# Optimization experiments

Hardware: AMD Instinct MI355X
Metric: run time of the kernel (lower is better)

The kernel has to match this reference:

```python
import jax, jax.numpy as jnp
import numpy as np

K_REGION = 32
C_CONTEXT = 128
CONF_THR = 0.5


def safe_normalize(x):
    return x / jnp.maximum(x.sum(axis=-1, keepdims=True), 1e-6)


def _geometry(mask_grid, h, w):
    # mask_grid: [B, K, h*w] -> per-mask bbox (x_min,y_min,x_max,y_max) + area, vectorized
    B, K, _ = mask_grid.shape
    m2 = mask_grid.reshape(B, K, h, w)
    present = m2 > 0.05
    rows = present.any(-1)  # [B,K,h]
    cols = present.any(-2)  # [B,K,w]
    yi = jnp.arange(h)
    xi = jnp.arange(w)
    y_min = jnp.min(jnp.where(rows, yi, h), axis=-1).astype(jnp.float32)
    y_max = jnp.max(jnp.where(rows, yi, -1), axis=-1).astype(jnp.float32)
    x_min = jnp.min(jnp.where(cols, xi, w), axis=-1).astype(jnp.float32)
    x_max = jnp.max(jnp.where(cols, xi, -1), axis=-1).astype(jnp.float32)
    hden = float(max(h - 1, 1))
    wden = float(max(w - 1, 1))
    area = present.astype(jnp.float32).mean(axis=(-1, -2))
    geom = jnp.stack([x_min / wden, y_min / hden, x_max / wden, y_max / hden, area], axis=-1)
    has_any = present.any(axis=(-1, -2))
    return jnp.where(has_any[..., None], geom, 0.0).astype(mask_grid.dtype)


def setup_inputs():
    key = jax.random.key(0)
    ks = jax.random.split(key, 16)
    B, N, D, M, Hm, Wm, Qd, Hd = 8, 576, 1024, 64, 384, 384, 4096, 1024
    inp = {}
    inp['patch_tokens'] = jax.random.normal(ks[0], (B, N, D), jnp.float32)
    inp['masks'] = jax.random.uniform(ks[1], (B, M, Hm, Wm), jnp.float32)
    inp['scores'] = jax.random.uniform(ks[2], (B, M), jnp.float32)
    inp['question_embed'] = jax.random.normal(ks[3], (B, Qd), jnp.float32)
    s = 0.02
    inp['W1'] = jax.random.normal(ks[4], (5, D), jnp.float32) * s
    inp['b1'] = jnp.zeros((D,), jnp.float32)
    inp['W2'] = jax.random.normal(ks[5], (D, D), jnp.float32) * s
    inp['b2'] = jnp.zeros((D,), jnp.float32)
    inp['Wv'] = jax.random.normal(ks[6], (D, Hd), jnp.float32) * s
    inp['bv'] = jnp.zeros((Hd,), jnp.float32)
    inp['Wp'] = jax.random.normal(ks[7], (1, Hd), jnp.float32) * s
    inp['bp'] = jnp.zeros((Hd,), jnp.float32)
    inp['Wq'] = jax.random.normal(ks[8], (Qd, Hd), jnp.float32) * s
    inp['bq'] = jnp.zeros((Hd,), jnp.float32)
    inp['Wo'] = jax.random.normal(ks[9], (Hd, 1), jnp.float32) * s
    inp['bo'] = jnp.zeros((1,), jnp.float32)
    inp['type_emb'] = jax.random.normal(ks[10], (3, D), jnp.float32) * s
    inp['patch_h'] = 24
    inp['patch_w'] = 24
    return inp


def reference(patch_tokens, masks, scores, question_embed, W1, b1, W2, b2,
              Wv, bv, Wp, bp, Wq, bq, Wo, bo, type_emb, patch_h, patch_w):
    B, N, D = patch_tokens.shape
    h, w = patch_h, patch_w
    M = masks.shape[1]

    grounding_valid = (masks.reshape(B, M, -1).sum(-1) > 0).any(-1)  # [B]

    order = jnp.argsort(-scores, axis=1)
    scores_s = jnp.take_along_axis(scores, order, axis=1)
    masks_s = jnp.take_along_axis(masks, order[:, :, None, None], axis=1)
    masks_k = masks_s[:, :K_REGION]
    scores_k = scores_s[:, :K_REGION]
    valid = scores_k >= CONF_THR
    masks_k = masks_k * valid[:, :, None, None].astype(masks_k.dtype)
    scores_k = jnp.where(valid, scores_k, 0.0)

    # MaskDownsampler: adaptive avg pool (exact: Hm,Wm divisible by h,w)
    Hm, Wm = masks_k.shape[-2:]
    fh, fw = Hm // h, Wm // w
    mg = masks_k.reshape(B, K_REGION, h, fh, w, fw).mean(axis=(3, 5)).reshape(B, K_REGION, h * w)

    uniform = jnp.full((B, K_REGION, N), 1.0 / N, dtype=patch_tokens.dtype)
    mg = jnp.where(grounding_valid[:, None, None], mg, uniform)
    scores_k = jnp.where(grounding_valid[:, None], scores_k, 1.0)

    # RegionPooler
    nm = safe_normalize(jnp.maximum(mg, 0.0))
    pooled = jnp.einsum('bkn,bnd->bkd', nm, patch_tokens)
    weighted = pooled * scores_k[..., None]
    geom = _geometry(mg, h, w)  # [B,K,5]
    g = jax.nn.silu(geom @ W1 + b1) @ W2 + b2
    region_tokens = weighted + g

    patch_prior = (mg * scores_k[..., None]).sum(axis=1)
    patch_prior = safe_normalize(jnp.maximum(patch_prior, 0.0))
    patch_prior = jnp.where(grounding_valid[:, None], patch_prior, jnp.full_like(patch_prior, 1.0 / N))

    # RoutingScorer
    hid = jnp.tanh(patch_tokens @ Wv + bv
                   + patch_prior[:, :, None] @ Wp + bp
                   + (question_embed @ Wq + bq)[:, None, :])
    routing_scores = (hid @ Wo + bo)[..., 0]  # [B,N]
    routing_weights = jax.nn.softmax(routing_scores, axis=-1)

    top_k = min(C_CONTEXT, N)
    _, sel_idx = jax.lax.top_k(routing_scores, top_k)
    context_tokens = jnp.take_along_axis(patch_tokens, sel_idx[:, :, None], axis=1)
    sel_mask = jnp.zeros((B, N), patch_tokens.dtype).at[jnp.arange(B)[:, None], sel_idx].set(1.0)

    # BackgroundPooler
    residual = jnp.maximum(1.0 - sel_mask, 0.0)
    residual = residual / jnp.maximum(residual.sum(-1, keepdims=True), 1e-6)
    bg = jnp.einsum('bn,bnd->bd', residual, patch_tokens)

    region_tokens = region_tokens + type_emb[0][None, None, :]
    context_tokens = context_tokens + type_emb[1][None, None, :]
    background_token = bg[:, None, :] + type_emb[2][None, None, :]
    visual_tokens = jnp.concatenate([region_tokens, context_tokens, background_token], axis=1)

    return (visual_tokens, region_tokens, context_tokens, background_token,
            patch_prior, routing_weights, sel_idx, grounding_valid)
```

## Files before the change

### kernel.cpp

```cpp
#include <hip/hip_runtime.h>
#include <math.h>

typedef long long I64;

#define NB    8
#define NTOK  576
#define DIM   1024
#define NMASK 64
#define HMASK 384
#define WMASK 384
#define QDIM  4096
#define HDIM  1024
#define KREG  32
#define CCTX  128
#define GH    24
#define GW    24
#define GNUM  576

#define OFF_VIS 0
#define OFF_REG 1318912
#define OFF_CTX 1581056
#define OFF_BG  2629632
#define OFF_PP  2637824
#define OFF_RW  2642432
#define OFF_SEL 2647040
#define OFF_GV  2648064

#define WS_BS   0
#define WS_NMAT 294912
#define WS_SCK  442368
#define WS_H1   442624
#define WS_Q    704768
#define WS_Q2   712960
#define WS_GV   721152
#define WS_PP   721160
#define WS_CS   725768
#define WS_RSP  733960

#define QBLK      256
#define BS_BLOCKS (NB * NMASK * 24)

__global__ __launch_bounds__(384) void k_bsq(const float* __restrict__ masks,
                                             const float* __restrict__ qe,
                                             const float* __restrict__ Wq,
                                             const float* __restrict__ bq,
                                             float* __restrict__ ws) {
  int gid = blockIdx.x;
  int t = threadIdx.x;
  __shared__ float shm[2048 + 6 * 64];
  if (gid >= QBLK) {
    int gid2 = gid - QBLK;
    int yband = gid2 % 24;
    int bm = gid2 / 24;
    float (*sm)[96] = (float(*)[96])shm;
    const float4* src = (const float4*)(masks + (I64)bm * (HMASK * WMASK) + (I64)yband * 16 * WMASK);
    float4 s4 = src[t];
    float4 v1 = src[t + 384];
    float4 v2 = src[t + 768];
    float4 v3 = src[t + 1152];
    s4.x += v1.x; s4.y += v1.y; s4.z += v1.z; s4.w += v1.w;
    s4.x += v2.x; s4.y += v2.y; s4.z += v2.z; s4.w += v2.w;
    s4.x += v3.x; s4.y += v3.y; s4.z += v3.z; s4.w += v3.w;
    float s = (s4.x + s4.y) + (s4.z + s4.w);
    sm[t / 96][t % 96] = s;
    __syncthreads();
    if (t < 24) {
      float tt = 0.f;
      #pragma unroll
      for (int rg = 0; rg < 4; ++rg)
        #pragma unroll
        for (int c = 0; c < 4; ++c) tt += sm[rg][t * 4 + c];
      ws[WS_BS + (I64)bm * GNUM + yband * 24 + t] = tt;
    }
  } else {
    int b = gid >> 5;
    int r = gid & 31;
    int qb = r >> 1;
    int ih = r & 1;
    int base = ih * 2048;
    float* qs = shm;
    float (*sp)[64] = (float(*)[64])(shm + 2048);
    {
      const float4* s4 = (const float4*)(qe + (I64)b * QDIM + base);
      float4 v = s4[t];
      *(float4*)&qs[t * 4] = v;
      if (t < 128) {
        float4 v2 = s4[t + 384];
        *(float4*)&qs[(t + 384) * 4] = v2;
      }
    }
    __syncthreads();
    int dl = t & 63, ig = t >> 6;
    int d = qb * 64 + dl;
    const float* wq = Wq + d;
    float a0 = 0.f, a1 = 0.f, a2 = 0.f, a3 = 0.f;
    float a4 = 0.f, a5 = 0.f, a6 = 0.f, a7 = 0.f;
    int i = ig;
    for (; i + 42 < 2048; i += 48) {
      a0 = fmaf(qs[i],      wq[(I64)(base + i) * HDIM],      a0);
      a1 = fmaf(qs[i + 6],  wq[(I64)(base + i + 6) * HDIM],  a1);
      a2 = fmaf(qs[i + 12], wq[(I64)(base + i + 12) * HDIM], a2);
      a3 = fmaf(qs[i + 18], wq[(I64)(base + i + 18) * HDIM], a3);
      a4 = fmaf(qs[i + 24], wq[(I64)(base + i + 24) * HDIM], a4);
      a5 = fmaf(qs[i + 30], wq[(I64)(base + i + 30) * HDIM], a5);
      a6 = fmaf(qs[i + 36], wq[(I64)(base + i + 36) * HDIM], a6);
      a7 = fmaf(qs[i + 42], wq[(I64)(base + i + 42) * HDIM], a7);
    }
    for (; i < 2048; i += 6)
      a0 = fmaf(qs[i], wq[(I64)(base + i) * HDIM], a0);
    sp[ig][dl] = ((a0 + a1) + (a2 + a3)) + ((a4 + a5) + (a6 + a7));
    __syncthreads();
    if (t < 64) {
      float s2 = ((sp[0][t] + sp[1][t]) + (sp[2][t] + sp[3][t])) + (sp[4][t] + sp[5][t]);
      int dd = qb * 64 + t;
      float outv = s2 + (ih ? 0.f : bq[dd]);
      ws[(ih ? WS_Q2 : WS_Q) + (I64)b * HDIM + dd] = outv;
    }
  }
}

#define MGPAD 580
__global__ __launch_bounds__(256) void k_perbatch(
    const float* __restrict__ bs, const float* __restrict__ scores,
    const float* __restrict__ W1, const float* __restrict__ b1,
    float* __restrict__ ws, float* __restrict__ out) {
  int b = blockIdx.x;
  int t = threadIdx.x;
  __shared__ float s_mg[KREG][MGPAD];
  __shared__ float s_sc[NMASK];
  __shared__ float s_msum[NMASK];
  __shared__ int   s_order[NMASK];
  __shared__ float s_sck[KREG];
  __shared__ int   s_valid[KREG];
  __shared__ int   s_midx[KREG];
  __shared__ float s_rowsum[KREG];
  __shared__ float s_pp[GNUM];
  __shared__ float s_geom[KREG][5];
  __shared__ float s_red[64];
  __shared__ int   s_gv;
  __shared__ float s_ppsum;

  {
    int m = t >> 2, q = t & 3;
    const float4* p = (const float4*)(bs + ((I64)b * NMASK + m) * GNUM) + q * 36;
    float s = 0.f;
    #pragma unroll 4
    for (int j = 0; j < 36; ++j) {
      float4 v = p[j];
      s += v.x; s += v.y; s += v.z; s += v.w;
    }
    s += __shfl_xor(s, 1);
    s += __shfl_xor(s, 2);
    if (q == 0) s_msum[m] = s;
  }
  if (t < NMASK) s_sc[t] = scores[b * NMASK + t];
  __syncthreads();
  if (t == 0) {
    int g = 0;
    for (int m = 0; m < NMASK; ++m) g |= (s_msum[m] > 0.f) ? 1 : 0;
    s_gv = g;
  }
  if (t < NMASK) {
    float v = s_sc[t];
    int r = 0;
    for (int j = 0; j < NMASK; ++j) {
      float vj = s_sc[j];
      r += (vj > v) || (vj == v && j < t);
    }
    s_order[r] = t;
  }
  __syncthreads();
  const int gv = s_gv;
  if (t < KREG) {
    int m = s_order[t];
    float sc = s_sc[m];
    int valid = (sc >= 0.5f) ? 1 : 0;
    s_midx[t] = m;
    s_valid[t] = valid;
    float sck = gv ? (valid ? sc : 0.f) : 1.f;
    s_sck[t] = sck;
    ws[WS_SCK + b * KREG + t] = sck;
  }
  __syncthreads();
  {
    int k = t >> 3, sub = t & 7;
    const float inv256 = 1.f / 256.f;
    const float invN = 1.f / 576.f;
    float scale = gv ? (s_valid[k] ? inv256 : 0.f) : 0.f;
    float addv  = gv ? 0.f : invN;
    const float4* src = (const float4*)(bs + ((I64)b * NMASK + s_midx[k]) * GNUM) + sub * 18;
    float* dst = &s_mg[k][sub * 72];
    #pragma unroll 3
    for (int j = 0; j < 18; ++j) {
      float4 v = src[j];
      v.x = v.x * scale + addv;
      v.y = v.y * scale + addv;
      v.z = v.z * scale + addv;
      v.w = v.w * scale + addv;
      *(float4*)(dst + j * 4) = v;
    }
  }
  __syncthreads();
  {
    int k = t >> 3, sub = t & 7;
    float part = 0.f;
    for (int n = sub; n < GNUM; n += 8) part += fmaxf(s_mg[k][n], 0.f);
    part += __shfl_xor(part, 1);
    part += __shfl_xor(part, 2);
    part += __shfl_xor(part, 4);
    if (sub == 0) s_rowsum[k] = part;
  }
  __syncthreads();
  for (int idx = t; idx < KREG * GNUM; idx += 256) {
    int k = idx / GNUM, n = idx - k * GNUM;
    float v = fmaxf(s_mg[k][n], 0.f);
    ws[WS_NMAT + ((I64)b * KREG + k) * GNUM + n] = v / fmaxf(s_rowsum[k], 1e-6f);
  }
  for (int n = t; n < GNUM; n += 256) {
    float raw = 0.f;
    #pragma unroll
    for (int k = 0; k < KREG; ++k) raw = fmaf(s_mg[k][n], s_sck[k], raw);
    s_pp[n] = fmaxf(raw, 0.f);
  }
  __syncthreads();
  if (t < 64) {
    float s = 0.f;
    for (int n = t; n < GNUM; n += 64) s += s_pp[n];
    s_red[t] = s;
  }
  __syncthreads();
  if (t == 0) {
    float s = 0.f;
    for (int i = 0; i < 64; ++i) s += s_red[i];
    s_ppsum = s;
  }
  __syncthreads();
  {
    const float invN = 1.f / 576.f;
    float den = fmaxf(s_ppsum, 1e-6f);
    for (int n = t; n < GNUM; n += 256) {
      float v = gv ? (s_pp[n] / den) : invN;
      ws[WS_PP + b * GNUM + n] = v;
      out[OFF_PP + b * GNUM + n] = v;
    }
  }
  {
    int k = t >> 3, sub = t & 7;
    unsigned colmask = 0u;
    int ymin = GH, ymax = -1, cnt = 0;
    #pragma unroll
    for (int yy = 0; yy < 3; ++yy) {
      int y = sub * 3 + yy;
      unsigned rowm = 0u;
      for (int x = 0; x < GW; ++x)
        if (s_mg[k][y * GW + x] > 0.05f) rowm |= (1u << x);
      if (rowm) { if (y < ymin) ymin = y; if (y > ymax) ymax = y; }
      colmask |= rowm;
      cnt += __popc(rowm);
    }
    #pragma unroll
    for (int off = 1; off < 8; off <<= 1) {
      colmask |= (unsigned)__shfl_xor((int)colmask, off);
      cnt += __shfl_xor(cnt, off);
      int o1 = __shfl_xor(ymin, off); ymin = (o1 < ymin) ? o1 : ymin;
      int o2 = __shfl_xor(ymax, off); ymax = (o2 > ymax) ? o2 : ymax;
    }
    if (sub == 0) {
      float g0, g1, g2, g3, g4;
      if (cnt > 0) {
        int xmin = __ffs(colmask) - 1;
        int xmax = 31 - __clz(colmask);
        g0 = (float)xmin / 23.f;
        g1 = (float)ymin / 23.f;
        g2 = (float)xmax / 23.f;
        g3 = (float)ymax / 23.f;
        g4 = (float)cnt / 576.f;
      } else { g0 = g1 = g2 = g3 = g4 = 0.f; }
      s_geom[k][0] = g0; s_geom[k][1] = g1; s_geom[k][2] = g2;
      s_geom[k][3] = g3; s_geom[k][4] = g4;
    }
  }
  __syncthreads();
  for (int idx = t; idx < KREG * HDIM; idx += 256) {
    int k = idx >> 10, j = idx & 1023;
    float x = 0.f;
    #pragma unroll
    for (int i = 0; i < 5; ++i) x += s_geom[k][i] * W1[i * HDIM + j];
    x += b1[j];
    float sg = 1.f / (1.f + expf(-x));
    ws[WS_H1 + ((I64)b * KREG + k) * HDIM + j] = x * sg;
  }
  if (t == 0) {
    float g = gv ? 1.f : 0.f;
    ws[WS_GV + b] = g;
    out[OFF_GV + b] = g;
  }
}

__global__ __launch_bounds__(512) void k_region(
    const float* __restrict__ pt, const float* __restrict__ W2,
    const float* __restrict__ b2, const float* __restrict__ te,
    float* __restrict__ ws, float* __restrict__ out) {
  int blk = blockIdx.x;
  int b = blk >> 6, kg = (blk >> 3) & 7, dg = blk & 7;
  int t = threadIdx.x;
  int dl = t & 127;
  int qh = t >> 7;
  int d = dg * 128 + dl;
  const float* nmb = ws + WS_NMAT + ((I64)b * KREG + kg * 4) * GNUM;
  const float* h1b = ws + WS_H1 + ((I64)b * KREG + kg * 4) * HDIM;
  float accP[4] = {0, 0, 0, 0};
  float accG[4] = {0, 0, 0, 0};
  float accS = 0.f;
  int n0 = qh * 144, n1 = n0 + 144;
  for (int n = n0; n < n1; ++n) {
    float p = pt[((I64)b * NTOK + n) * DIM + d];
    accS += p;
    #pragma unroll
    for (int kk = 0; kk < 4; ++kk)
      accP[kk] = fmaf(nmb[kk * GNUM + n], p, accP[kk]);
  }
  int j0 = qh * 256, j1 = j0 + 256;
  for (int j = j0; j < j1; ++j) {
    float wv = W2[(I64)j * DIM + d];
    #pragma unroll
    for (int kk = 0; kk < 4; ++kk)
      accG[kk] = fmaf(h1b[kk * HDIM + j], wv, accG[kk]);
  }
  __shared__ float cmbP[4][4][128];
  __shared__ float cmbG[4][4][128];
  __shared__ float cmbS[4][128];
  #pragma unroll
  for (int kk = 0; kk < 4; ++kk) {
    cmbP[qh][kk][dl] = accP[kk];
    cmbG[qh][kk][dl] = accG[kk];
  }
  cmbS[qh][dl] = accS;
  __syncthreads();
  if (qh == 0) {
    float bb = b2[d], t0 = te[d];
    #pragma unroll
    for (int kk = 0; kk < 4; ++kk) {
      int k = kg * 4 + kk;
      float P = (cmbP[0][kk][dl] + cmbP[1][kk][dl]) + (cmbP[2][kk][dl] + cmbP[3][kk][dl]);
      float G = (cmbG[0][kk][dl] + cmbG[1][kk][dl]) + (cmbG[2][kk][dl] + cmbG[3][kk][dl]);
      float val = P * ws[WS_SCK + b * KREG + k] + G + bb + t0;
      out[OFF_REG + ((I64)b * KREG + k) * DIM + d] = val;
      out[OFF_VIS + ((I64)b * 161 + k) * DIM + d] = val;
    }
    if (kg == 0)
      ws[WS_CS + (I64)b * DIM + d] =
          (cmbS[0][dl] + cmbS[1][dl]) + (cmbS[2][dl] + cmbS[3][dl]);
  }
}

#define PA 36
#define PW 164
__global__ __launch_bounds__(256, 1) void k_hid4(
    const float* __restrict__ pt, const float* __restrict__ Wv,
    const float* __restrict__ bv, const float* __restrict__ Wp,
    const float* __restrict__ bp, const float* __restrict__ Wo,
    float* __restrict__ ws) {
  int blk = blockIdx.x;
  int b = blk >> 5;
  int r = blk & 31;
  int tokTile = r >> 3;
  int colTile = r & 7;
  int n0 = tokTile * 144;
  int col0 = colTile * 128;
  int t = threadIdx.x;
  int trow = t >> 4;
  int tcol = t & 15;

  __shared__ float sA[2][144][PA];
  __shared__ float sW[2][32][PW];

  float acc[9][8];
  #pragma unroll
  for (int i = 0; i < 9; ++i)
    #pragma unroll
    for (int j = 0; j < 8; ++j) acc[i][j] = 0.f;

  int a_row0 = t >> 3, a_kq0 = t & 7;
  int a_row1 = (t + 256) >> 3, a_kq1 = t & 7;
  int a_row2 = (t + 512) >> 3;
  int a_row3 = (t + 768) >> 3;
  int a_row4 = (t + 1024) >> 3;
  int w_k0 = t >> 5, w_c = t & 31;

  float4 pa0, pa1, pa2, pa3, pa4;
  float4 pw0, pw1, pw2, pw3;

  const float* ptb = pt + (I64)(b * NTOK + n0) * DIM;
  const float* wvb = Wv + col0;

  {
    pa0 = *(const float4*)&ptb[(I64)a_row0 * DIM + a_kq0 * 4];
    pa1 = *(const float4*)&ptb[(I64)a_row1 * DIM + a_kq1 * 4];
    pa2 = *(const float4*)&ptb[(I64)a_row2 * DIM + a_kq1 * 4];
    pa3 = *(const float4*)&ptb[(I64)a_row3 * DIM + a_kq1 * 4];
    if (t < 128) pa4 = *(const float4*)&ptb[(I64)a_row4 * DIM + a_kq1 * 4];
    pw0 = *(const float4*)&wvb[(I64)(w_k0 +  0) * HDIM + w_c * 4];
    pw1 = *(const float4*)&wvb[(I64)(w_k0 +  8) * HDIM + w_c * 4];
    pw2 = *(const float4*)&wvb[(I64)(w_k0 + 16) * HDIM + w_c * 4];
    pw3 = *(const float4*)&wvb[(I64)(w_k0 + 24) * HDIM + w_c * 4];
    *(float4*)&sA[0][a_row0][a_kq0 * 4] = pa0;
    *(float4*)&sA[0][a_row1][a_kq1 * 4] = pa1;
    *(float4*)&sA[0][a_row2][a_kq1 * 4] = pa2;
    *(float4*)&sA[0][a_row3][a_kq1 * 4] = pa3;
    if (t < 128) *(float4*)&sA[0][a_row4][a_kq1 * 4] = pa4;
    *(float4*)&sW[0][w_k0 +  0][w_c * 4] = pw0;
    *(float4*)&sW[0][w_k0 +  8][w_c * 4] = pw1;
    *(float4*)&sW[0][w_k0 + 16][w_c * 4] = pw2;
    *(float4*)&sW[0][w_k0 + 24][w_c * 4] = pw3;
  }

  for (int s = 0; s < 32; ++s) {
    __syncthreads();
    if (s + 1 < 32) {
      int k0 = (s + 1) * 32;
      pa0 = *(const float4*)&ptb[(I64)a_row0 * DIM + k0 + a_kq0 * 4];
      pa1 = *(const float4*)&ptb[(I64)a_row1 * DIM + k0 + a_kq1 * 4];
      pa2 = *(const float4*)&ptb[(I64)a_row2 * DIM + k0 + a_kq1 * 4];
      pa3 = *(const float4*)&ptb[(I64)a_row3 * DIM + k0 + a_kq1 * 4];
      if (t < 128) pa4 = *(const float4*)&ptb[(I64)a_row4 * DIM + k0 + a_kq1 * 4];
      pw0 = *(const float4*)&wvb[(I64)(k0 + w_k0 +  0) * HDIM + w_c * 4];
      pw1 = *(const float4*)&wvb[(I64)(k0 + w_k0 +  8) * HDIM + w_c * 4];
      pw2 = *(const float4*)&wvb[(I64)(k0 + w_k0 + 16) * HDIM + w_c * 4];
      pw3 = *(const float4*)&wvb[(I64)(k0 + w_k0 + 24) * HDIM + w_c * 4];
    }
    int cur = s & 1;
    #pragma unroll 2
    for (int kk4 = 0; kk4 < 8; ++kk4) {
      float4 af[9];
      #pragma unroll
      for (int i = 0; i < 9; ++i)
        af[i] = *(const float4*)&sA[cur][trow * 9 + i][kk4 * 4];
      float4 w0[4], w1[4];
      #pragma unroll
      for (int m = 0; m < 4; ++m) {
        w0[m] = *(const float4*)&sW[cur][kk4 * 4 + m][tcol * 4];
        w1[m] = *(const float4*)&sW[cur][kk4 * 4 + m][64 + tcol * 4];
      }
      #pragma unroll
      for (int i = 0; i < 9; ++i) {
        #pragma unroll
        for (int m = 0; m < 4; ++m) {
          float a = ((const float*)&af[i])[m];
          acc[i][0] = fmaf(a, w0[m].x, acc[i][0]);
          acc[i][1] = fmaf(a, w0[m].y, acc[i][1]);
          acc[i][2] = fmaf(a, w0[m].z, acc[i][2]);
          acc[i][3] = fmaf(a, w0[m].w, acc[i][3]);
          acc[i][4] = fmaf(a, w1[m].x, acc[i][4]);
          acc[i][5] = fmaf(a, w1[m].y, acc[i][5]);
          acc[i][6] = fmaf(a, w1[m].z, acc[i][6]);
          acc[i][7] = fmaf(a, w1[m].w, acc[i][7]);
        }
      }
    }
    if (s + 1 < 32) {
      int nxt = (s + 1) & 1;
      *(float4*)&sA[nxt][a_row0][a_kq0 * 4] = pa0;
      *(float4*)&sA[nxt][a_row1][a_kq1 * 4] = pa1;
      *(float4*)&sA[nxt][a_row2][a_kq1 * 4] = pa2;
      *(float4*)&sA[nxt][a_row3][a_kq1 * 4] = pa3;
      if (t < 128) *(float4*)&sA[nxt][a_row4][a_kq1 * 4] = pa4;
      *(float4*)&sW[nxt][w_k0 +  0][w_c * 4] = pw0;
      *(float4*)&sW[nxt][w_k0 +  8][w_c * 4] = pw1;
      *(float4*)&sW[nxt][w_k0 + 16][w_c * 4] = pw2;
      *(float4*)&sW[nxt][w_k0 + 24][w_c * 4] = pw3;
    }
  }

  int ca = col0 + tcol * 4;
  int cb = col0 + 64 + tcol * 4;
  float4 bvA = *(const float4*)&bv[ca], bvB = *(const float4*)&bv[cb];
  float4 bpA = *(const float4*)&bp[ca], bpB = *(const float4*)&bp[cb];
  float4 wpA = *(const float4*)&Wp[ca], wpB = *(const float4*)&Wp[cb];
  float4 woA = *(const float4*)&Wo[ca], woB = *(const float4*)&Wo[cb];
  float4 qaA = *(const float4*)&ws[WS_Q  + (I64)b * HDIM + ca];
  float4 qaB = *(const float4*)&ws[WS_Q  + (I64)b * HDIM + cb];
  float4 qbA = *(const float4*)&ws[WS_Q2 + (I64)b * HDIM + ca];
  float4 qbB = *(const float4*)&ws[WS_Q2 + (I64)b * HDIM + cb];
  float bvv[8] = {bvA.x, bvA.y, bvA.z, bvA.w, bvB.x, bvB.y, bvB.z, bvB.w};
  float bpv[8] = {bpA.x, bpA.y, bpA.z, bpA.w, bpB.x, bpB.y, bpB.z, bpB.w};
  float wpv[8] = {wpA.x, wpA.y, wpA.z, wpA.w, wpB.x, wpB.y, wpB.z, wpB.w};
  float wov[8] = {woA.x, woA.y, woA.z, woA.w, woB.x, woB.y, woB.z, woB.w};
  float qv[8]  = {qaA.x + qbA.x, qaA.y + qbA.y, qaA.z + qbA.z, qaA.w + qbA.w,
                  qaB.x + qbB.x, qaB.y + qbB.y, qaB.z + qbB.z, qaB.w + qbB.w};
  float partial[9];
  #pragma unroll
  for (int i = 0; i < 9; ++i) {
    float ppv = ws[WS_PP + b * GNUM + n0 + trow * 9 + i];
    float s = 0.f;
    #pragma unroll
    for (int j = 0; j < 8; ++j) {
      float pre = acc[i][j] + bvv[j] + bpv[j] + qv[j] + ppv * wpv[j];
      s = fmaf(wov[j], tanhf(pre), s);
    }
    partial[i] = s;
  }
  #pragma unroll
  for (int i = 0; i < 9; ++i) {
    float p = partial[i];
    p += __shfl_xor(p, 1);
    p += __shfl_xor(p, 2);
    p += __shfl_xor(p, 4);
    p += __shfl_xor(p, 8);
    partial[i] = p;
  }
  if (tcol == 0) {
    #pragma unroll
    for (int i = 0; i < 9; ++i)
      ws[WS_RSP + ((I64)b * NTOK + n0 + trow * 9 + i) * 8 + colTile] = partial[i];
  }
}

__global__ __launch_bounds__(576) void k_soft(const float* __restrict__ bo,
                                              float* __restrict__ ws, float* __restrict__ out) {
  int b = blockIdx.x, t = threadIdx.x;
  __shared__ float s_rs[NTOK];
  __shared__ float s_w[9];
  __shared__ float s_max, s_sum;
  {
    const float4* p = (const float4*)(ws + WS_RSP + ((I64)b * NTOK + t) * 8);
    float4 v0 = p[0], v1 = p[1];
    s_rs[t] = bo[0] + (((v0.x + v0.y) + (v0.z + v0.w)) + ((v1.x + v1.y) + (v1.z + v1.w)));
  }
  __syncthreads();
  float v = s_rs[t];
  int r = 0;
  for (int j = 0; j < NTOK; ++j) {
    float vj = s_rs[j];
    r += (vj > v) || (vj == v && j < t);
  }
  float m = v;
  for (int off = 1; off < 64; off <<= 1) m = fmaxf(m, __shfl_xor(m, off));
  if ((t & 63) == 0) s_w[t >> 6] = m;
  __syncthreads();
  if (t == 0) {
    float mm = s_w[0];
    for (int i = 1; i < 9; ++i) mm = fmaxf(mm, s_w[i]);
    s_max = mm;
  }
  __syncthreads();
  float e = expf(v - s_max);
  float s = e;
  for (int off = 1; off < 64; off <<= 1) s += __shfl_xor(s, off);
  if ((t & 63) == 0) s_w[t >> 6] = s;
  __syncthreads();
  if (t == 0) {
    float ss = 0.f;
    for (int i = 0; i < 9; ++i) ss += s_w[i];
    s_sum = ss;
  }
  __syncthreads();
  out[OFF_RW + b * NTOK + t] = e / s_sum;
  if (r < CCTX) out[OFF_SEL + b * CCTX + r] = (float)t;
}

__global__ __launch_bounds__(256) void k_post(const float* __restrict__ pt, const float* __restrict__ te,
                                              const float* __restrict__ ws, const float* __restrict__ outr,
                                              float* __restrict__ out) {
  int rr = blockIdx.x, b = blockIdx.y;
  int d = threadIdx.x * 4;
  if (rr < CCTX) {
    int idx = (int)outr[OFF_SEL + b * CCTX + rr];
    float4 v = *(const float4*)&pt[((I64)b * NTOK + idx) * DIM + d];
    float4 e = *(const float4*)&te[DIM + d];
    v.x += e.x; v.y += e.y; v.z += e.z; v.w += e.w;
    *(float4*)&out[OFF_CTX + ((I64)b * CCTX + rr) * DIM + d] = v;
    *(float4*)&out[OFF_VIS + ((I64)b * 161 + KREG + rr) * DIM + d] = v;
  } else {
    float4 s = *(const float4*)&ws[WS_CS + (I64)b * DIM + d];
    for (int r = 0; r < CCTX; ++r) {
      int idx = (int)outr[OFF_SEL + b * CCTX + r];
      float4 v = *(const float4*)&pt[((I64)b * NTOK + idx) * DIM + d];
      s.x -= v.x; s.y -= v.y; s.z -= v.z; s.w -= v.w;
    }
    const float rinv = 1.f / 448.f;
    float4 e = *(const float4*)&te[2 * DIM + d];
    float4 o;
    o.x = s.x * rinv + e.x; o.y = s.y * rinv + e.y;
    o.z = s.z * rinv + e.z; o.w = s.w * rinv + e.w;
    *(float4*)&out[OFF_BG + (I64)b * DIM + d] = o;
    *(float4*)&out[OFF_VIS + ((I64)b * 161 + 160) * DIM + d] = o;
  }
}

extern "C" void kernel_launch(void* const* d_in, const int* in_sizes, int n_in,
                              void* d_out, int out_size, void* d_ws, size_t ws_size,
                              hipStream_t stream) {
  (void)in_sizes; (void)n_in; (void)out_size; (void)ws_size;
  const float* pt     = (const float*)d_in[0];
  const float* masks  = (const float*)d_in[1];
  const float* scores = (const float*)d_in[2];
  const float* qe     = (const float*)d_in[3];
  const float* W1     = (const float*)d_in[4];
  const float* b1     = (const float*)d_in[5];
  const float* W2     = (const float*)d_in[6];
  const float* b2     = (const float*)d_in[7];
  const float* Wv     = (const float*)d_in[8];
  const float* bv     = (const float*)d_in[9];
  const float* Wp     = (const float*)d_in[10];
  const float* bp     = (const float*)d_in[11];
  const float* Wq     = (const float*)d_in[12];
  const float* bq     = (const float*)d_in[13];
  const float* Wo     = (const float*)d_in[14];
  const float* bo     = (const float*)d_in[15];
  const float* te     = (const float*)d_in[16];
  float* out = (float*)d_out;
  float* ws  = (float*)d_ws;

  k_bsq<<<dim3(QBLK + BS_BLOCKS), dim3(384), 0, stream>>>(masks, qe, Wq, bq, ws);
  k_perbatch<<<dim3(NB), dim3(256), 0, stream>>>(ws + WS_BS, scores, W1, b1, ws, out);
  k_region<<<dim3(512), dim3(512), 0, stream>>>(pt, W2, b2, te, ws, out);
  k_hid4<<<dim3(256), dim3(256), 0, stream>>>(pt, Wv, bv, Wp, bp, Wo, ws);
  k_soft<<<dim3(NB), dim3(576), 0, stream>>>(bo, ws, out);
  k_post<<<dim3(CCTX + 1, NB), dim3(256), 0, stream>>>(pt, te, ws, out, out);
}
```

Measured before the change: 343.2 us.

## Fold hidden GEMM into mask/query megakernel and split tanh epilogue into region kernel

The Wv GEMM moves into the first launch alongside the mask band sums and the question projection. It no longer depends on patch_prior, so it can overlap those independent stages, and it writes the raw hidden matrix to workspace. The tanh/Wo epilogue, which needs patch_prior, is appended as extra blocks in the region kernel, and softmax then reads finished routing scores. The GEMM drops LDS double buffering so three blocks can fit per CU, and the background pooling gather is split across four thread groups. The cost is an extra ~19MB hidden-state write and read through workspace.

```diff
diff --git a/kernel.cpp b/kernel.cpp
--- a/kernel.cpp
+++ b/kernel.cpp
@@ -35,86 +35,183 @@
 #define WS_GV   721152
 #define WS_PP   721160
 #define WS_CS   725768
-#define WS_RSP  733960
+#define WS_RS   733960
+#define WS_HID  775432
+#define WS_END  5494024
 
 #define QBLK      256
 #define BS_BLOCKS (NB * NMASK * 24)
-
-__global__ __launch_bounds__(384) void k_bsq(const float* __restrict__ masks,
-                                             const float* __restrict__ qe,
-                                             const float* __restrict__ Wq,
-                                             const float* __restrict__ bq,
-                                             float* __restrict__ ws) {
+#define HIDBLK    256
+#define MEGA_GRID (HIDBLK + QBLK + BS_BLOCKS)
+
+__global__ __launch_bounds__(256, 3) void k_mega(
+    const float* __restrict__ masks, const float* __restrict__ qe,
+    const float* __restrict__ Wq, const float* __restrict__ bq,
+    const float* __restrict__ pt, const float* __restrict__ Wv,
+    float* __restrict__ ws) {
   int gid = blockIdx.x;
   int t = threadIdx.x;
-  __shared__ float shm[2048 + 6 * 64];
-  if (gid >= QBLK) {
-    int gid2 = gid - QBLK;
-    int yband = gid2 % 24;
-    int bm = gid2 / 24;
-    float (*sm)[96] = (float(*)[96])shm;
-    const float4* src = (const float4*)(masks + (I64)bm * (HMASK * WMASK) + (I64)yband * 16 * WMASK);
-    float4 s4 = src[t];
-    float4 v1 = src[t + 384];
-    float4 v2 = src[t + 768];
-    float4 v3 = src[t + 1152];
-    s4.x += v1.x; s4.y += v1.y; s4.z += v1.z; s4.w += v1.w;
-    s4.x += v2.x; s4.y += v2.y; s4.z += v2.z; s4.w += v2.w;
-    s4.x += v3.x; s4.y += v3.y; s4.z += v3.z; s4.w += v3.w;
-    float s = (s4.x + s4.y) + (s4.z + s4.w);
-    sm[t / 96][t % 96] = s;
-    __syncthreads();
-    if (t < 24) {
-      float tt = 0.f;
-      #pragma unroll
-      for (int rg = 0; rg < 4; ++rg)
-        #pragma unroll
-        for (int c = 0; c < 4; ++c) tt += sm[rg][t * 4 + c];
-      ws[WS_BS + (I64)bm * GNUM + yband * 24 + t] = tt;
-    }
-  } else {
+  __shared__ __align__(16) float smem[10432];
+
+  if (gid < HIDBLK) {
     int b = gid >> 5;
     int r = gid & 31;
-    int qb = r >> 1;
-    int ih = r & 1;
+    int tokTile = r >> 3;
+    int colTile = r & 7;
+    int n0 = tokTile * 144;
+    int col0 = colTile * 128;
+    int trow = t >> 4;
+    int tcol = t & 15;
+
+    float (*sA)[36]  = (float(*)[36])smem;
+    float (*sW)[164] = (float(*)[164])(smem + 5184);
+
+    float acc[9][8];
+    #pragma unroll
+    for (int i = 0; i < 9; ++i)
+      #pragma unroll
+      for (int j = 0; j < 8; ++j) acc[i][j] = 0.f;
+
+    int a_row0 = t >> 3, a_kq = t & 7;
+    int a_row1 = (t + 256) >> 3;
+    int a_row2 = (t + 512) >> 3;
+    int a_row3 = (t + 768) >> 3;
+    int a_row4 = (t + 1024) >> 3;
+    int w_k0 = t >> 5, w_c = t & 31;
+
+    const float* ptb = pt + (I64)(b * NTOK + n0) * DIM;
+    const float* wvb = Wv + col0;
+
+    float4 pa0, pa1, pa2, pa3, pa4 = {0,0,0,0};
+    float4 pw0, pw1, pw2, pw3;
+
+    pa0 = *(const float4*)&ptb[(I64)a_row0 * DIM + a_kq * 4];
+    pa1 = *(const float4*)&ptb[(I64)a_row1 * DIM + a_kq * 4];
+    pa2 = *(const float4*)&ptb[(I64)a_row2 * DIM + a_kq * 4];
+    pa3 = *(const float4*)&ptb[(I64)a_row3 * DIM + a_kq * 4];
+    if (t < 128) pa4 = *(const float4*)&ptb[(I64)a_row4 * DIM + a_kq * 4];
+    pw0 = *(const float4*)&wvb[(I64)(w_k0 +  0) * HDIM + w_c * 4];
+    pw1 = *(const float4*)&wvb[(I64)(w_k0 +  8) * HDIM + w_c * 4];
+    pw2 = *(const float4*)&wvb[(I64)(w_k0 + 16) * HDIM + w_c * 4];
+    pw3 = *(const float4*)&wvb[(I64)(w_k0 + 24) * HDIM + w_c * 4];
+
+    for (int s = 0; s < 32; ++s) {
+      __syncthreads();
+      *(float4*)&sA[a_row0][a_kq * 4] = pa0;
+      *(float4*)&sA[a_row1][a_kq * 4] = pa1;
+      *(float4*)&sA[a_row2][a_kq * 4] = pa2;
+      *(float4*)&sA[a_row3][a_kq * 4] = pa3;
+      if (t < 128) *(float4*)&sA[a_row4][a_kq * 4] = pa4;
+      *(float4*)&sW[w_k0 +  0][w_c * 4] = pw0;
+      *(float4*)&sW[w_k0 +  8][w_c * 4] = pw1;
+      *(float4*)&sW[w_k0 + 16][w_c * 4] = pw2;
+      *(float4*)&sW[w_k0 + 24][w_c * 4] = pw3;
+      __syncthreads();
+      if (s + 1 < 32) {
+        int k0 = (s + 1) * 32;
+        pa0 = *(const float4*)&ptb[(I64)a_row0 * DIM + k0 + a_kq * 4];
+        pa1 = *(const float4*)&ptb[(I64)a_row1 * DIM + k0 + a_kq * 4];
+        pa2 = *(const float4*)&ptb[(I64)a_row2 * DIM + k0 + a_kq * 4];
+        pa3 = *(const float4*)&ptb[(I64)a_row3 * DIM + k0 + a_kq * 4];
+        if (t < 128) pa4 = *(const float4*)&ptb[(I64)a_row4 * DIM + k0 + a_kq * 4];
+        pw0 = *(const float4*)&wvb[(I64)(k0 + w_k0 +  0) * HDIM + w_c * 4];
+        pw1 = *(const float4*)&wvb[(I64)(k0 + w_k0 +  8) * HDIM + w_c * 4];
+        pw2 = *(const float4*)&wvb[(I64)(k0 + w_k0 + 16) * HDIM + w_c * 4];
+        pw3 = *(const float4*)&wvb[(I64)(k0 + w_k0 + 24) * HDIM + w_c * 4];
+      }
+      __builtin_amdgcn_s_setprio(1);
+      #pragma unroll 2
+      for (int kk4 = 0; kk4 < 8; ++kk4) {
+        float4 af[9];
+        #pragma unroll
+        for (int i = 0; i < 9; ++i)
+          af[i] = *(const float4*)&sA[trow * 9 + i][kk4 * 4];
+        float4 w0[4], w1[4];
+        #pragma unroll
+        for (int m = 0; m < 4; ++m) {
+          w0[m] = *(const float4*)&sW[kk4 * 4 + m][tcol * 4];
+          w1[m] = *(const float4*)&sW[kk4 * 4 + m][64 + tcol * 4];
+        }
+        #pragma unroll
+        for (int i = 0; i < 9; ++i) {
+          #pragma unroll
+          for (int m = 0; m < 4; ++m) {
+            float a = ((const float*)&af[i])[m];
+            acc[i][0] = fmaf(a, w0[m].x, acc[i][0]);
+            acc[i][1] = fmaf(a, w0[m].y, acc[i][1]);
+            acc[i][2] = fmaf(a, w0[m].z, acc[i][2]);
+            acc[i][3] = fmaf(a, w0[m].w, acc[i][3]);
+            acc[i][4] = fmaf(a, w1[m].x, acc[i][4]);
+            acc[i][5] = fmaf(a, w1[m].y, acc[i][5]);
+            acc[i][6] = fmaf(a, w1[m].z, acc[i][6]);
+            acc[i][7] = fmaf(a, w1[m].w, acc[i][7]);
+          }
+        }
+      }
+      __builtin_amdgcn_s_setprio(0);
+    }
+    float* hid = ws + WS_HID + ((I64)b * NTOK + n0) * HDIM;
+    #pragma unroll
+    for (int i = 0; i < 9; ++i) {
+      int row = trow * 9 + i;
+      float4 va = {acc[i][0], acc[i][1], acc[i][2], acc[i][3]};
+      float4 vb = {acc[i][4], acc[i][5], acc[i][6], acc[i][7]};
+      *(float4*)&hid[(I64)row * HDIM + col0 + tcol * 4] = va;
+      *(float4*)&hid[(I64)row * HDIM + col0 + 64 + tcol * 4] = vb;
+    }
+  } else if (gid < HIDBLK + QBLK) {
+    int g = gid - HIDBLK;
+    int b = g >> 5, r = g & 31;
+    int qb = r >> 1, ih = r & 1;
     int base = ih * 2048;
-    float* qs = shm;
-    float (*sp)[64] = (float(*)[64])(shm + 2048);
-    {
-      const float4* s4 = (const float4*)(qe + (I64)b * QDIM + base);
-      float4 v = s4[t];
-      *(float4*)&qs[t * 4] = v;
-      if (t < 128) {
-        float4 v2 = s4[t + 384];
-        *(float4*)&qs[(t + 384) * 4] = v2;
-      }
-    }
+    float* qs = smem;
+    float (*sp)[64] = (float(*)[64])(smem + 2048);
+    const float4* s4 = (const float4*)(qe + (I64)b * QDIM + base);
+    *(float4*)&qs[t * 4] = s4[t];
+    *(float4*)&qs[(t + 256) * 4] = s4[t + 256];
     __syncthreads();
     int dl = t & 63, ig = t >> 6;
     int d = qb * 64 + dl;
     const float* wq = Wq + d;
     float a0 = 0.f, a1 = 0.f, a2 = 0.f, a3 = 0.f;
     float a4 = 0.f, a5 = 0.f, a6 = 0.f, a7 = 0.f;
-    int i = ig;
-    for (; i + 42 < 2048; i += 48) {
+    for (int i = ig; i < 2048; i += 32) {
       a0 = fmaf(qs[i],      wq[(I64)(base + i) * HDIM],      a0);
-      a1 = fmaf(qs[i + 6],  wq[(I64)(base + i + 6) * HDIM],  a1);
-      a2 = fmaf(qs[i + 12], wq[(I64)(base + i + 12) * HDIM], a2);
-      a3 = fmaf(qs[i + 18], wq[(I64)(base + i + 18) * HDIM], a3);
-      a4 = fmaf(qs[i + 24], wq[(I64)(base + i + 24) * HDIM], a4);
-      a5 = fmaf(qs[i + 30], wq[(I64)(base + i + 30) * HDIM], a5);
-      a6 = fmaf(qs[i + 36], wq[(I64)(base + i + 36) * HDIM], a6);
-      a7 = fmaf(qs[i + 42], wq[(I64)(base + i + 42) * HDIM], a7);
-    }
-    for (; i < 2048; i += 6)
-      a0 = fmaf(qs[i], wq[(I64)(base + i) * HDIM], a0);
+      a1 = fmaf(qs[i + 4],  wq[(I64)(base + i + 4) * HDIM],  a1);
+      a2 = fmaf(qs[i + 8],  wq[(I64)(base + i + 8) * HDIM],  a2);
+      a3 = fmaf(qs[i + 12], wq[(I64)(base + i + 12) * HDIM], a3);
+      a4 = fmaf(qs[i + 16], wq[(I64)(base + i + 16) * HDIM], a4);
+      a5 = fmaf(qs[i + 20], wq[(I64)(base + i + 20) * HDIM], a5);
+      a6 = fmaf(qs[i + 24], wq[(I64)(base + i + 24) * HDIM], a6);
+      a7 = fmaf(qs[i + 28], wq[(I64)(base + i + 28) * HDIM], a7);
+    }
     sp[ig][dl] = ((a0 + a1) + (a2 + a3)) + ((a4 + a5) + (a6 + a7));
     __syncthreads();
     if (t < 64) {
-      float s2 = ((sp[0][t] + sp[1][t]) + (sp[2][t] + sp[3][t])) + (sp[4][t] + sp[5][t]);
+      float s2 = (sp[0][t] + sp[1][t]) + (sp[2][t] + sp[3][t]);
       int dd = qb * 64 + t;
-      float outv = s2 + (ih ? 0.f : bq[dd]);
-      ws[(ih ? WS_Q2 : WS_Q) + (I64)b * HDIM + dd] = outv;
+      ws[(ih ? WS_Q2 : WS_Q) + (I64)b * HDIM + dd] = s2 + (ih ? 0.f : bq[dd]);
+    }
+  } else {
+    int g = gid - (HIDBLK + QBLK);
+    int yband = g % 24;
+    int bm = g / 24;
+    float (*sm)[96] = (float(*)[96])smem;
+    const float4* src = (const float4*)(masks + (I64)bm * (HMASK * WMASK) + (I64)yband * 16 * WMASK);
+    #pragma unroll
+    for (int j = 0; j < 6; ++j) {
+      int f = t + 256 * j;
+      float4 v = src[f];
+      sm[f / 96][f % 96] = (v.x + v.y) + (v.z + v.w);
+    }
+    __syncthreads();
+    if (t < 24) {
+      float tt = 0.f;
+      #pragma unroll
+      for (int rr = 0; rr < 16; ++rr)
+        #pragma unroll
+        for (int c = 0; c < 4; ++c) tt += sm[rr][t * 4 + c];
+      ws[WS_BS + (I64)bm * GNUM + yband * 24 + t] = tt;
     }
   }
 }
@@ -297,236 +394,103 @@
   }
 }
 
-__global__ __launch_bounds__(512) void k_region(
+__global__ __launch_bounds__(512) void k_regepi(
     const float* __restrict__ pt, const float* __restrict__ W2,
     const float* __restrict__ b2, const float* __restrict__ te,
+    const float* __restrict__ bv, const float* __restrict__ bp,
+    const float* __restrict__ Wp, const float* __restrict__ Wo,
+    const float* __restrict__ bo,
     float* __restrict__ ws, float* __restrict__ out) {
   int blk = blockIdx.x;
-  int b = blk >> 6, kg = (blk >> 3) & 7, dg = blk & 7;
   int t = threadIdx.x;
-  int dl = t & 127;
-  int qh = t >> 7;
-  int d = dg * 128 + dl;
-  const float* nmb = ws + WS_NMAT + ((I64)b * KREG + kg * 4) * GNUM;
-  const float* h1b = ws + WS_H1 + ((I64)b * KREG + kg * 4) * HDIM;
-  float accP[4] = {0, 0, 0, 0};
-  float accG[4] = {0, 0, 0, 0};
-  float accS = 0.f;
-  int n0 = qh * 144, n1 = n0 + 144;
-  for (int n = n0; n < n1; ++n) {
-    float p = pt[((I64)b * NTOK + n) * DIM + d];
-    accS += p;
-    #pragma unroll
-    for (int kk = 0; kk < 4; ++kk)
-      accP[kk] = fmaf(nmb[kk * GNUM + n], p, accP[kk]);
-  }
-  int j0 = qh * 256, j1 = j0 + 256;
-  for (int j = j0; j < j1; ++j) {
-    float wv = W2[(I64)j * DIM + d];
-    #pragma unroll
-    for (int kk = 0; kk < 4; ++kk)
-      accG[kk] = fmaf(h1b[kk * HDIM + j], wv, accG[kk]);
-  }
-  __shared__ float cmbP[4][4][128];
-  __shared__ float cmbG[4][4][128];
-  __shared__ float cmbS[4][128];
-  #pragma unroll
-  for (int kk = 0; kk < 4; ++kk) {
-    cmbP[qh][kk][dl] = accP[kk];
-    cmbG[qh][kk][dl] = accG[kk];
-  }
-  cmbS[qh][dl] = accS;
-  __syncthreads();
-  if (qh == 0) {
-    float bb = b2[d], t0 = te[d];
+  if (blk < 512) {
+    int b = blk >> 6, kg = (blk >> 3) & 7, dg = blk & 7;
+    int dl = t & 127;
+    int qh = t >> 7;
+    int d = dg * 128 + dl;
+    const float* nmb = ws + WS_NMAT + ((I64)b * KREG + kg * 4) * GNUM;
+    const float* h1b = ws + WS_H1 + ((I64)b * KREG + kg * 4) * HDIM;
+    float accP[4] = {0, 0, 0, 0};
+    float accG[4] = {0, 0, 0, 0};
+    float accS = 0.f;
+    int n0 = qh * 144, n1 = n0 + 144;
+    for (int n = n0; n < n1; ++n) {
+      float p = pt[((I64)b * NTOK + n) * DIM + d];
+      accS += p;
+      #pragma unroll
+      for (int kk = 0; kk < 4; ++kk)
+        accP[kk] = fmaf(nmb[kk * GNUM + n], p, accP[kk]);
+    }
+    int j0 = qh * 256, j1 = j0 + 256;
+    for (int j = j0; j < j1; ++j) {
+      float wv = W2[(I64)j * DIM + d];
+      #pragma unroll
+      for (int kk = 0; kk < 4; ++kk)
+        accG[kk] = fmaf(h1b[kk * HDIM + j], wv, accG[kk]);
+    }
+    __shared__ float cmbP[4][4][128];
+    __shared__ float cmbG[4][4][128];
+    __shared__ float cmbS[4][128];
     #pragma unroll
     for (int kk = 0; kk < 4; ++kk) {
-      int k = kg * 4 + kk;
-      float P = (cmbP[0][kk][dl] + cmbP[1][kk][dl]) + (cmbP[2][kk][dl] + cmbP[3][kk][dl]);
-      float G = (cmbG[0][kk][dl] + cmbG[1][kk][dl]) + (cmbG[2][kk][dl] + cmbG[3][kk][dl]);
-      float val = P * ws[WS_SCK + b * KREG + k] + G + bb + t0;
-      out[OFF_REG + ((I64)b * KREG + k) * DIM + d] = val;
-      out[OFF_VIS + ((I64)b * 161 + k) * DIM + d] = val;
-    }
-    if (kg == 0)
-      ws[WS_CS + (I64)b * DIM + d] =
-          (cmbS[0][dl] + cmbS[1][dl]) + (cmbS[2][dl] + cmbS[3][dl]);
+      cmbP[qh][kk][dl] = accP[kk];
+      cmbG[qh][kk][dl] = accG[kk];
+    }
+    cmbS[qh][dl] = accS;
+    __syncthreads();
+    if (qh == 0) {
+      float bb = b2[d], t0 = te[d];
+      #pragma unroll
+      for (int kk = 0; kk < 4; ++kk) {
+        int k = kg * 4 + kk;
+        float P = (cmbP[0][kk][dl] + cmbP[1][kk][dl]) + (cmbP[2][kk][dl] + cmbP[3][kk][dl]);
+        float G = (cmbG[0][kk][dl] + cmbG[1][kk][dl]) + (cmbG[2][kk][dl] + cmbG[3][kk][dl]);
+        float val = P * ws[WS_SCK + b * KREG + k] + G + bb + t0;
+        out[OFF_REG + ((I64)b * KREG + k) * DIM + d] = val;
+        out[OFF_VIS + ((I64)b * 161 + k) * DIM + d] = val;
+      }
+      if (kg == 0)
+        ws[WS_CS + (I64)b * DIM + d] =
+            (cmbS[0][dl] + cmbS[1][dl]) + (cmbS[2][dl] + cmbS[3][dl]);
+    }
+  } else {
+    int g = (blk - 512) * 32 + (t >> 4);
+    int l = t & 15;
+    int b = g / NTOK, n = g % NTOK;
+    const float* hid = ws + WS_HID + (I64)g * HDIM;
+    const float* q1 = ws + WS_Q + (I64)b * HDIM;
+    const float* q2 = ws + WS_Q2 + (I64)b * HDIM;
+    float ppv = ws[WS_PP + b * GNUM + n];
+    float ssum = 0.f;
+    #pragma unroll 4
+    for (int j = 0; j < 16; ++j) {
+      int c = l * 64 + j * 4;
+      float4 h4 = *(const float4*)&hid[c];
+      float4 b4 = *(const float4*)&bv[c];
+      float4 p4 = *(const float4*)&bp[c];
+      float4 w4 = *(const float4*)&Wp[c];
+      float4 o4 = *(const float4*)&Wo[c];
+      float4 qa = *(const float4*)&q1[c];
+      float4 qb = *(const float4*)&q2[c];
+      ssum = fmaf(o4.x, tanhf(h4.x + b4.x + p4.x + qa.x + qb.x + ppv * w4.x), ssum);
+      ssum = fmaf(o4.y, tanhf(h4.y + b4.y + p4.y + qa.y + qb.y + ppv * w4.y), ssum);
+      ssum = fmaf(o4.z, tanhf(h4.z + b4.z + p4.z + qa.z + qb.z + ppv * w4.z), ssum);
+      ssum = fmaf(o4.w, tanhf(h4.w + b4.w + p4.w + qa.w + qb.w + ppv * w4.w), ssum);
+    }
+    ssum += __shfl_xor(ssum, 1);
+    ssum += __shfl_xor(ssum, 2);
+    ssum += __shfl_xor(ssum, 4);
+    ssum += __shfl_xor(ssum, 8);
+    if (l == 0) ws[WS_RS + g] = ssum + bo[0];
   }
 }
 
-#define PA 36
-#define PW 164
-__global__ __launch_bounds__(256, 1) void k_hid4(
-    const float* __restrict__ pt, const float* __restrict__ Wv,
-    const float* __restrict__ bv, const float* __restrict__ Wp,
-    const float* __restrict__ bp, const float* __restrict__ Wo,
-    float* __restrict__ ws) {
-  int blk = blockIdx.x;
-  int b = blk >> 5;
-  int r = blk & 31;
-  int tokTile = r >> 3;
-  int colTile = r & 7;
-  int n0 = tokTile * 144;
-  int col0 = colTile * 128;
-  int t = threadIdx.x;
-  int trow = t >> 4;
-  int tcol = t & 15;
-
-  __shared__ float sA[2][144][PA];
-  __shared__ float sW[2][32][PW];
-
-  float acc[9][8];
-  #pragma unroll
-  for (int i = 0; i < 9; ++i)
-    #pragma unroll
-    for (int j = 0; j < 8; ++j) acc[i][j] = 0.f;
-
-  int a_row0 = t >> 3, a_kq0 = t & 7;
-  int a_row1 = (t + 256) >> 3, a_kq1 = t & 7;
-  int a_row2 = (t + 512) >> 3;
-  int a_row3 = (t + 768) >> 3;
-  int a_row4 = (t + 1024) >> 3;
-  int w_k0 = t >> 5, w_c = t & 31;
-
-  float4 pa0, pa1, pa2, pa3, pa4;
-  float4 pw0, pw1, pw2, pw3;
-
-  const float* ptb = pt + (I64)(b * NTOK + n0) * DIM;
-  const float* wvb = Wv + col0;
-
-  {
-    pa0 = *(const float4*)&ptb[(I64)a_row0 * DIM + a_kq0 * 4];
-    pa1 = *(const float4*)&ptb[(I64)a_row1 * DIM + a_kq1 * 4];
-    pa2 = *(const float4*)&ptb[(I64)a_row2 * DIM + a_kq1 * 4];
-    pa3 = *(const float4*)&ptb[(I64)a_row3 * DIM + a_kq1 * 4];
-    if (t < 128) pa4 = *(const float4*)&ptb[(I64)a_row4 * DIM + a_kq1 * 4];
-    pw0 = *(const float4*)&wvb[(I64)(w_k0 +  0) * HDIM + w_c * 4];
-    pw1 = *(const float4*)&wvb[(I64)(w_k0 +  8) * HDIM + w_c * 4];
-    pw2 = *(const float4*)&wvb[(I64)(w_k0 + 16) * HDIM + w_c * 4];
-    pw3 = *(const float4*)&wvb[(I64)(w_k0 + 24) * HDIM + w_c * 4];
-    *(float4*)&sA[0][a_row0][a_kq0 * 4] = pa0;
-    *(float4*)&sA[0][a_row1][a_kq1 * 4] = pa1;
-    *(float4*)&sA[0][a_row2][a_kq1 * 4] = pa2;
-    *(float4*)&sA[0][a_row3][a_kq1 * 4] = pa3;
-    if (t < 128) *(float4*)&sA[0][a_row4][a_kq1 * 4] = pa4;
-    *(float4*)&sW[0][w_k0 +  0][w_c * 4] = pw0;
-    *(float4*)&sW[0][w_k0 +  8][w_c * 4] = pw1;
-    *(float4*)&sW[0][w_k0 + 16][w_c * 4] = pw2;
-    *(float4*)&sW[0][w_k0 + 24][w_c * 4] = pw3;
-  }
-
-  for (int s = 0; s < 32; ++s) {
-    __syncthreads();
-    if (s + 1 < 32) {
-      int k0 = (s + 1) * 32;
-      pa0 = *(const float4*)&ptb[(I64)a_row0 * DIM + k0 + a_kq0 * 4];
-      pa1 = *(const float4*)&ptb[(I64)a_row1 * DIM + k0 + a_kq1 * 4];
-      pa2 = *(const float4*)&ptb[(I64)a_row2 * DIM + k0 + a_kq1 * 4];
-      pa3 = *(const float4*)&ptb[(I64)a_row3 * DIM + k0 + a_kq1 * 4];
-      if (t < 128) pa4 = *(const float4*)&ptb[(I64)a_row4 * DIM + k0 + a_kq1 * 4];
-      pw0 = *(const float4*)&wvb[(I64)(k0 + w_k0 +  0) * HDIM + w_c * 4];
-      pw1 = *(const float4*)&wvb[(I64)(k0 + w_k0 +  8) * HDIM + w_c * 4];
-      pw2 = *(const float4*)&wvb[(I64)(k0 + w_k0 + 16) * HDIM + w_c * 4];
-      pw3 = *(const float4*)&wvb[(I64)(k0 + w_k0 + 24) * HDIM + w_c * 4];
-    }
-    int cur = s & 1;
-    #pragma unroll 2
-    for (int kk4 = 0; kk4 < 8; ++kk4) {
-      float4 af[9];
-      #pragma unroll
-      for (int i = 0; i < 9; ++i)
-        af[i] = *(const float4*)&sA[cur][trow * 9 + i][kk4 * 4];
-      float4 w0[4], w1[4];
-      #pragma unroll
-      for (int m = 0; m < 4; ++m) {
-        w0[m] = *(const float4*)&sW[cur][kk4 * 4 + m][tcol * 4];
-        w1[m] = *(const float4*)&sW[cur][kk4 * 4 + m][64 + tcol * 4];
-      }
-      #pragma unroll
-      for (int i = 0; i < 9; ++i) {
-        #pragma unroll
-        for (int m = 0; m < 4; ++m) {
-          float a = ((const float*)&af[i])[m];
-          acc[i][0] = fmaf(a, w0[m].x, acc[i][0]);
-          acc[i][1] = fmaf(a, w0[m].y, acc[i][1]);
-          acc[i][2] = fmaf(a, w0[m].z, acc[i][2]);
-          acc[i][3] = fmaf(a, w0[m].w, acc[i][3]);
-          acc[i][4] = fmaf(a, w1[m].x, acc[i][4]);
-          acc[i][5] = fmaf(a, w1[m].y, acc[i][5]);
-          acc[i][6] = fmaf(a, w1[m].z, acc[i][6]);
-          acc[i][7] = fmaf(a, w1[m].w, acc[i][7]);
-        }
-      }
-    }
-    if (s + 1 < 32) {
-      int nxt = (s + 1) & 1;
-      *(float4*)&sA[nxt][a_row0][a_kq0 * 4] = pa0;
-      *(float4*)&sA[nxt][a_row1][a_kq1 * 4] = pa1;
-      *(float4*)&sA[nxt][a_row2][a_kq1 * 4] = pa2;
-      *(float4*)&sA[nxt][a_row3][a_kq1 * 4] = pa3;
-      if (t < 128) *(float4*)&sA[nxt][a_row4][a_kq1 * 4] = pa4;
-      *(float4*)&sW[nxt][w_k0 +  0][w_c * 4] = pw0;
-      *(float4*)&sW[nxt][w_k0 +  8][w_c * 4] = pw1;
-      *(float4*)&sW[nxt][w_k0 + 16][w_c * 4] = pw2;
-      *(float4*)&sW[nxt][w_k0 + 24][w_c * 4] = pw3;
-    }
-  }
-
-  int ca = col0 + tcol * 4;
-  int cb = col0 + 64 + tcol * 4;
-  float4 bvA = *(const float4*)&bv[ca], bvB = *(const float4*)&bv[cb];
-  float4 bpA = *(const float4*)&bp[ca], bpB = *(const float4*)&bp[cb];
-  float4 wpA = *(const float4*)&Wp[ca], wpB = *(const float4*)&Wp[cb];
-  float4 woA = *(const float4*)&Wo[ca], woB = *(const float4*)&Wo[cb];
-  float4 qaA = *(const float4*)&ws[WS_Q  + (I64)b * HDIM + ca];
-  float4 qaB = *(const float4*)&ws[WS_Q  + (I64)b * HDIM + cb];
-  float4 qbA = *(const float4*)&ws[WS_Q2 + (I64)b * HDIM + ca];
-  float4 qbB = *(const float4*)&ws[WS_Q2 + (I64)b * HDIM + cb];
-  float bvv[8] = {bvA.x, bvA.y, bvA.z, bvA.w, bvB.x, bvB.y, bvB.z, bvB.w};
-  float bpv[8] = {bpA.x, bpA.y, bpA.z, bpA.w, bpB.x, bpB.y, bpB.z, bpB.w};
-  float wpv[8] = {wpA.x, wpA.y, wpA.z, wpA.w, wpB.x, wpB.y, wpB.z, wpB.w};
-  float wov[8] = {woA.x, woA.y, woA.z, woA.w, woB.x, woB.y, woB.z, woB.w};
-  float qv[8]  = {qaA.x + qbA.x, qaA.y + qbA.y, qaA.z + qbA.z, qaA.w + qbA.w,
-                  qaB.x + qbB.x, qaB.y + qbB.y, qaB.z + qbB.z, qaB.w + qbB.w};
-  float partial[9];
-  #pragma unroll
-  for (int i = 0; i < 9; ++i) {
-    float ppv = ws[WS_PP + b * GNUM + n0 + trow * 9 + i];
-    float s = 0.f;
-    #pragma unroll
-    for (int j = 0; j < 8; ++j) {
-      float pre = acc[i][j] + bvv[j] + bpv[j] + qv[j] + ppv * wpv[j];
-      s = fmaf(wov[j], tanhf(pre), s);
-    }
-    partial[i] = s;
-  }
-  #pragma unroll
-  for (int i = 0; i < 9; ++i) {
-    float p = partial[i];
-    p += __shfl_xor(p, 1);
-    p += __shfl_xor(p, 2);
-    p += __shfl_xor(p, 4);
-    p += __shfl_xor(p, 8);
-    partial[i] = p;
-  }
-  if (tcol == 0) {
-    #pragma unroll
-    for (int i = 0; i < 9; ++i)
-      ws[WS_RSP + ((I64)b * NTOK + n0 + trow * 9 + i) * 8 + colTile] = partial[i];
-  }
-}
-
-__global__ __launch_bounds__(576) void k_soft(const float* __restrict__ bo,
-                                              float* __restrict__ ws, float* __restrict__ out) {
+__global__ __launch_bounds__(576) void k_soft2(float* __restrict__ ws, float* __restrict__ out) {
   int b = blockIdx.x, t = threadIdx.x;
   __shared__ float s_rs[NTOK];
   __shared__ float s_w[9];
   __shared__ float s_max, s_sum;
-  {
-    const float4* p = (const float4*)(ws + WS_RSP + ((I64)b * NTOK + t) * 8);
-    float4 v0 = p[0], v1 = p[1];
-    s_rs[t] = bo[0] + (((v0.x + v0.y) + (v0.z + v0.w)) + ((v1.x + v1.y) + (v1.z + v1.w)));
-  }
+  s_rs[t] = ws[WS_RS + b * NTOK + t];
   __syncthreads();
   float v = s_rs[t];
   int r = 0;
@@ -563,8 +527,8 @@
                                               const float* __restrict__ ws, const float* __restrict__ outr,
                                               float* __restrict__ out) {
   int rr = blockIdx.x, b = blockIdx.y;
-  int d = threadIdx.x * 4;
   if (rr < CCTX) {
+    int d = threadIdx.x * 4;
     int idx = (int)outr[OFF_SEL + b * CCTX + rr];
     float4 v = *(const float4*)&pt[((I64)b * NTOK + idx) * DIM + d];
     float4 e = *(const float4*)&te[DIM + d];
@@ -572,19 +536,35 @@
     *(float4*)&out[OFF_CTX + ((I64)b * CCTX + rr) * DIM + d] = v;
     *(float4*)&out[OFF_VIS + ((I64)b * 161 + KREG + rr) * DIM + d] = v;
   } else {
-    float4 s = *(const float4*)&ws[WS_CS + (I64)b * DIM + d];
-    for (int r = 0; r < CCTX; ++r) {
-      int idx = (int)outr[OFF_SEL + b * CCTX + r];
-      float4 v = *(const float4*)&pt[((I64)b * NTOK + idx) * DIM + d];
-      s.x -= v.x; s.y -= v.y; s.z -= v.z; s.w -= v.w;
-    }
-    const float rinv = 1.f / 448.f;
-    float4 e = *(const float4*)&te[2 * DIM + d];
-    float4 o;
-    o.x = s.x * rinv + e.x; o.y = s.y * rinv + e.y;
-    o.z = s.z * rinv + e.z; o.w = s.w * rinv + e.w;
-    *(float4*)&out[OFF_BG + (I64)b * DIM + d] = o;
-    *(float4*)&out[OFF_VIS + ((I64)b * 161 + 160) * DIM + d] = o;
+    int dl = threadIdx.x & 63;
+    int rg = threadIdx.x >> 6;
+    __shared__ float4 cmb[4][64];
+    #pragma unroll
+    for (int dd = 0; dd < 4; ++dd) {
+      int d = (dd * 64 + dl) * 4;
+      float4 s = {0.f, 0.f, 0.f, 0.f};
+      for (int r = rg * 32; r < rg * 32 + 32; ++r) {
+        int idx = (int)outr[OFF_SEL + b * CCTX + r];
+        float4 v = *(const float4*)&pt[((I64)b * NTOK + idx) * DIM + d];
+        s.x += v.x; s.y += v.y; s.z += v.z; s.w += v.w;
+      }
+      cmb[rg][dl] = s;
+      __syncthreads();
+      if (rg == 0) {
+        float4 s0 = cmb[0][dl], s1 = cmb[1][dl], s2 = cmb[2][dl], s3 = cmb[3][dl];
+        float4 cs = *(const float4*)&ws[WS_CS + (I64)b * DIM + d];
+        const float rinv = 1.f / 448.f;
+        float4 e = *(const float4*)&te[2 * DIM + d];
+        float4 o;
+        o.x = (cs.x - ((s0.x + s1.x) + (s2.x + s3.x))) * rinv + e.x;
+        o.y = (cs.y - ((s0.y + s1.y) + (s2.y + s3.y))) * rinv + e.y;
+        o.z = (cs.z - ((s0.z + s1.z) + (s2.z + s3.z))) * rinv + e.z;
+        o.w = (cs.w - ((s0.w + s1.w) + (s2.w + s3.w))) * rinv + e.w;
+        *(float4*)&out[OFF_BG + (I64)b * DIM + d] = o;
+        *(float4*)&out[OFF_VIS + ((I64)b * 161 + 160) * DIM + d] = o;
+      }
+      __syncthreads();
+    }
   }
 }
 
@@ -612,10 +592,9 @@
   float* out = (float*)d_out;
   float* ws  = (float*)d_ws;
 
-  k_bsq<<<dim3(QBLK + BS_BLOCKS), dim3(384), 0, stream>>>(masks, qe, Wq, bq, ws);
+  k_mega<<<dim3(MEGA_GRID), dim3(256), 0, stream>>>(masks, qe, Wq, bq, pt, Wv, ws);
   k_perbatch<<<dim3(NB), dim3(256), 0, stream>>>(ws + WS_BS, scores, W1, b1, ws, out);
-  k_region<<<dim3(512), dim3(512), 0, stream>>>(pt, W2, b2, te, ws, out);
-  k_hid4<<<dim3(256), dim3(256), 0, stream>>>(pt, Wv, bv, Wp, bp, Wo, ws);
-  k_soft<<<dim3(NB), dim3(576), 0, stream>>>(bo, ws, out);
+  k_regepi<<<dim3(512 + 144), dim3(512), 0, stream>>>(pt, W2, b2, te, bv, bp, Wp, Wo, bo, ws, out);
+  k_soft2<<<dim3(NB), dim3(576), 0, stream>>>(ws, out);
   k_post<<<dim3(CCTX + 1, NB), dim3(256), 0, stream>>>(pt, te, ws, out, out);
 }
```

Result: slower. 434.4 us (+26.6%).
